# Performance work log

Measured on AMD Instinct MI355X. Metric: run time of the kernel, lower is better.

Reference implementation:

```python
import jax, jax.numpy as jnp
import numpy as np

H = 8
NEG = -1e9


def setup_inputs() -> dict:
    key = jax.random.key(0)
    ks = jax.random.split(key, 16)
    B, S, D = 4, 512, 512
    dk = D // H
    NUM_REL = 20 * 2 + 1  # 41
    s_in = 1.0 / np.sqrt(D)
    s_emb = np.sqrt(6.0 / (NUM_REL + dk))  # xavier_uniform
    inp = {
        "query": jax.random.normal(ks[0], (B, S, D), jnp.float32),
        "key": jax.random.normal(ks[1], (B, S, D), jnp.float32),
        "value": jax.random.normal(ks[2], (B, S, D), jnp.float32),
        "mask": jax.random.randint(ks[3], (B, S, S), 0, NUM_REL, jnp.int32),
        # linear layers stored as [in, out] (y = x @ W + b)
        "Wq": jax.random.normal(ks[4], (D, D), jnp.float32) * s_in,
        "bq": jnp.zeros((D,), jnp.float32),
        "Wk": jax.random.normal(ks[5], (D, D), jnp.float32) * s_in,
        "bk": jnp.zeros((D,), jnp.float32),
        "Wv": jax.random.normal(ks[6], (D, D), jnp.float32) * s_in,
        "bv": jnp.zeros((D,), jnp.float32),
        "Wo": jax.random.normal(ks[7], (D, D), jnp.float32) * s_in,
        "bo": jnp.zeros((D,), jnp.float32),
        "emb_k": jax.random.uniform(ks[8], (NUM_REL, dk), jnp.float32, -s_emb, s_emb),
        "emb_v": jax.random.uniform(ks[9], (NUM_REL, dk), jnp.float32, -s_emb, s_emb),
    }
    return inp


def reference(query, key, value, mask, Wq, bq, Wk, bk, Wv, bv, Wo, bo, emb_k, emb_v):
    B, Q, D = query.shape
    K = key.shape[1]
    dk = D // H
    # project and split heads -> [B, H, S, dk]
    q = (query @ Wq + bq).reshape(B, Q, H, dk).transpose(0, 2, 1, 3)
    k = (key @ Wk + bk).reshape(B, K, H, dk).transpose(0, 2, 1, 3)
    v = (value @ Wv + bv).reshape(B, K, H, dk).transpose(0, 2, 1, 3)
    # gather relative-position embeddings: [B, Q, K, dk]
    relem = emb_k[mask]
    relemv = emb_v[mask]
    scale = 1.0 / jnp.sqrt(jnp.asarray(dk, q.dtype))
    # content scores + relative-position bias scores
    scores = (jnp.einsum("bhqd,bhkd->bhqk", q, k)
              + jnp.einsum("bhqd,bqkd->bhqk", q, relem)) * scale
    # rmask = (mask > 0), broadcast over heads
    scores = jnp.where((mask > 0)[:, None, :, :], scores, NEG)
    attn = jax.nn.softmax(scores, axis=-1)
    # content values + relative-position value bias
    x = (jnp.einsum("bhqk,bhkd->bhqd", attn, v)
         + jnp.einsum("bhqk,bqkd->bhqd", attn, relemv))
    x = x.transpose(0, 2, 1, 3).reshape(B, Q, D)
    return x @ Wo + bo
```

## Files before the change

kernel.cpp:

```cpp
#include <hip/hip_runtime.h>

#define B_ 4
#define S_ 512
#define D_ 512
#define H_ 8
#define DK_ 64
#define NREL 41

typedef __attribute__((ext_vector_type(8))) short bf16x8;
typedef __attribute__((ext_vector_type(4))) float f32x4;

__device__ __forceinline__ unsigned short f2bf(float f) {
  unsigned u = __float_as_uint(f);
  u = u + 0x7FFFu + ((u >> 16) & 1u);
  return (unsigned short)(u >> 16);
}

#define MFMA16(a, b, c) __builtin_amdgcn_mfma_f32_16x16x32_bf16((a), (b), (c), 0, 0, 0)

struct PrepArgs { const float* W[4]; const float* in[3]; };

__global__ __launch_bounds__(256) void prep(PrepArgs PA,
    const float* __restrict__ embk, const float* __restrict__ embv,
    ushort* __restrict__ WT0, ushort* __restrict__ ekb, ushort* __restrict__ evt,
    ushort* __restrict__ inbf0)
{
  const int z = blockIdx.z;
  const int t = threadIdx.x;
  if (z == 4) {
    if (blockIdx.x || blockIdx.y) return;
    for (int i = t; i < 48 * 64; i += 256) {
      int r = i >> 6, d = i & 63;
      ekb[i] = (r < NREL) ? f2bf(embk[r * 64 + d]) : (ushort)0;
    }
    for (int i = t; i < 64 * 64; i += 256) {
      int d = i >> 6, r = i & 63;
      evt[i] = (r < NREL) ? f2bf(embv[r * 64 + d]) : (ushort)0;
    }
    return;
  }
  if (z >= 5) {
    const float* src = PA.in[z - 5];
    ushort* dst = inbf0 + (size_t)(z - 5) * ((size_t)2048 * 512);
    int lb = blockIdx.y * 8 + blockIdx.x;
    size_t base = (size_t)lb * 16384;
    #pragma unroll
    for (int i = 0; i < 16; ++i) {
      size_t off = base + (size_t)i * 1024 + t * 4;
      float4 v = *(const float4*)&src[off];
      ushort4 pk;
      pk.x = f2bf(v.x); pk.y = f2bf(v.y); pk.z = f2bf(v.z); pk.w = f2bf(v.w);
      *(ushort4*)&dst[off] = pk;
    }
    return;
  }
  __shared__ float sh[64][65];
  const float* W = PA.W[z];
  ushort* WT = WT0 + (size_t)z * (D_ * D_);
  const int k0 = blockIdx.x * 64, n0 = blockIdx.y * 64;
  const int rr = t >> 4, cc = (t & 15) * 4;
  #pragma unroll
  for (int i = 0; i < 4; ++i) {
    float4 v = *(const float4*)&W[(size_t)(k0 + rr + i * 16) * D_ + n0 + cc];
    sh[rr + i * 16][cc + 0] = v.x; sh[rr + i * 16][cc + 1] = v.y;
    sh[rr + i * 16][cc + 2] = v.z; sh[rr + i * 16][cc + 3] = v.w;
  }
  __syncthreads();
  #pragma unroll
  for (int i = 0; i < 4; ++i) {
    int r2 = rr + i * 16;
    ushort4 pk;
    pk.x = f2bf(sh[cc + 0][r2]); pk.y = f2bf(sh[cc + 1][r2]);
    pk.z = f2bf(sh[cc + 2][r2]); pk.w = f2bf(sh[cc + 3][r2]);
    *(ushort4*)&WT[(size_t)(n0 + r2) * D_ + k0 + cc] = pk;
  }
}

struct GemmP  { const ushort* A; const ushort* Wt; const float* bias; void* out; int mode; int kbeg; int kend; };
struct GemmPs { GemmP p[3]; };

__global__ __launch_bounds__(256) void gemm_bf16(GemmPs P)
{
  __shared__ ushort As[64][72];
  __shared__ ushort Bs[64][72];
  const GemmP gp = P.p[blockIdx.z];
  const int t = threadIdx.x, l = t & 63, w = t >> 6;
  const int r16 = l & 15, g4 = l >> 4;
  const int wmo = (w >> 1) * 32, wno = (w & 1) * 32;
  const int m0 = blockIdx.x * 64, n0 = blockIdx.y * 64;

  f32x4 acc[2][2];
  #pragma unroll
  for (int mi = 0; mi < 2; ++mi)
    #pragma unroll
    for (int ni = 0; ni < 2; ++ni) acc[mi][ni] = 0.0f;

  const int srow = t >> 2, sseg = (t & 3) * 16;
  for (int k0 = gp.kbeg; k0 < gp.kend; k0 += 64) {
    __syncthreads();
    *(uint4*)&As[srow][sseg]     = *(const uint4*)&gp.A[(size_t)(m0 + srow) * D_ + k0 + sseg];
    *(uint4*)&As[srow][sseg + 8] = *(const uint4*)&gp.A[(size_t)(m0 + srow) * D_ + k0 + sseg + 8];
    *(uint4*)&Bs[srow][sseg]     = *(const uint4*)&gp.Wt[(size_t)(n0 + srow) * D_ + k0 + sseg];
    *(uint4*)&Bs[srow][sseg + 8] = *(const uint4*)&gp.Wt[(size_t)(n0 + srow) * D_ + k0 + sseg + 8];
    __syncthreads();
    #pragma unroll
    for (int kk = 0; kk < 2; ++kk) {
      bf16x8 af[2], bfr[2];
      #pragma unroll
      for (int i = 0; i < 2; ++i) af[i]  = *(const bf16x8*)&As[wmo + i * 16 + r16][kk * 32 + g4 * 8];
      #pragma unroll
      for (int i = 0; i < 2; ++i) bfr[i] = *(const bf16x8*)&Bs[wno + i * 16 + r16][kk * 32 + g4 * 8];
      #pragma unroll
      for (int mi = 0; mi < 2; ++mi)
        #pragma unroll
        for (int ni = 0; ni < 2; ++ni)
          acc[mi][ni] = MFMA16(af[mi], bfr[ni], acc[mi][ni]);
    }
  }

  #pragma unroll
  for (int mi = 0; mi < 2; ++mi) {
    #pragma unroll
    for (int ni = 0; ni < 2; ++ni) {
      int n = n0 + wno + ni * 16 + r16;
      int mb = m0 + wmo + mi * 16 + g4 * 4;
      if (gp.mode == 3) {
        float* PO = (float*)gp.out;
        #pragma unroll
        for (int r = 0; r < 4; ++r) PO[(size_t)(mb + r) * D_ + n] = acc[mi][ni][r];
      } else {
        float bv = gp.bias[n];
        ushort* O = (ushort*)gp.out;
        int h = n >> 6, d = n & 63;
        if (gp.mode == 1) {
          #pragma unroll
          for (int r = 0; r < 4; ++r) {
            int m = mb + r, b = m >> 9, s = m & 511;
            O[(((size_t)(b * H_ + h)) * S_ + s) * DK_ + d] = f2bf(acc[mi][ni][r] + bv);
          }
        } else {
          int b = mb >> 9, s = mb & 511;
          ushort4 pk;
          pk.x = f2bf(acc[mi][ni][0] + bv); pk.y = f2bf(acc[mi][ni][1] + bv);
          pk.z = f2bf(acc[mi][ni][2] + bv); pk.w = f2bf(acc[mi][ni][3] + bv);
          *(ushort4*)&O[(((size_t)(b * H_ + h)) * DK_ + d) * S_ + s] = pk;
        }
      }
    }
  }
}

__global__ __launch_bounds__(64) void attn_mfma(
    const ushort* __restrict__ qb,
    const ushort* __restrict__ kb,
    const ushort* __restrict__ vtb,
    const int*    __restrict__ mask,
    const ushort* __restrict__ ekb,
    const ushort* __restrict__ evt,
    float* __restrict__ part,
    float* __restrict__ sums)
{
  __shared__ ushort Pb[16][72];
  __shared__ float qrel[16][48];
  __shared__ float wr[16][64];

  const int l = threadIdx.x;
  const int g = blockIdx.x;
  const int h = g & 7, b = (g >> 3) & 3;
  const int rest = g >> 5;
  const int chunk = rest & 3, qt = rest >> 2;
  const int bh = b * H_ + h;
  const int r16 = l & 15, g4 = l >> 4;

  for (int i = l; i < 16 * 64; i += 64) (&wr[0][0])[i] = 0.f;

  const size_t qoff = ((size_t)bh * S_ + qt * 16) * DK_;
  bf16x8 qf0 = *(const bf16x8*)&qb[qoff + (size_t)r16 * DK_ + g4 * 8];
  bf16x8 qf1 = *(const bf16x8*)&qb[qoff + (size_t)r16 * DK_ + 32 + g4 * 8];

  {
    #pragma unroll
    for (int s = 0; s < 3; ++s) {
      bf16x8 e0 = *(const bf16x8*)&ekb[(s * 16 + r16) * 64 + g4 * 8];
      bf16x8 e1 = *(const bf16x8*)&ekb[(s * 16 + r16) * 64 + 32 + g4 * 8];
      f32x4 qr = 0.0f;
      qr = MFMA16(qf0, e0, qr);
      qr = MFMA16(qf1, e1, qr);
      #pragma unroll
      for (int r = 0; r < 4; ++r) qrel[g4 * 4 + r][s * 16 + r16] = qr[r];
    }
  }
  __syncthreads();

  float ssum[4] = {0.f, 0.f, 0.f, 0.f};
  f32x4 oacc[4];
  #pragma unroll
  for (int i = 0; i < 4; ++i) oacc[i] = 0.0f;

  const int* mbase = mask + ((size_t)b * S_ + qt * 16) * S_;
  const size_t voff = (size_t)bh * DK_ * S_;

  const int kt0 = chunk * 2;
  for (int kt = kt0; kt < kt0 + 2; ++kt) {
    const size_t koff = ((size_t)bh * S_ + kt * 64) * DK_;
    f32x4 sacc[4];
    #pragma unroll
    for (int sub = 0; sub < 4; ++sub) {
      bf16x8 kf0 = *(const bf16x8*)&kb[koff + (size_t)(sub * 16 + r16) * DK_ + g4 * 8];
      bf16x8 kf1 = *(const bf16x8*)&kb[koff + (size_t)(sub * 16 + r16) * DK_ + 32 + g4 * 8];
      f32x4 z = 0.0f;
      z = MFMA16(qf0, kf0, z);
      z = MFMA16(qf1, kf1, z);
      sacc[sub] = z;
    }
    #pragma unroll
    for (int sub = 0; sub < 4; ++sub) {
      #pragma unroll
      for (int r = 0; r < 4; ++r) {
        int row = g4 * 4 + r;
        int col = kt * 64 + sub * 16 + r16;
        int mv = mbase[(size_t)row * S_ + col];
        float sc = (sacc[sub][r] + qrel[row][mv]) * 0.125f;
        float e = (mv > 0) ? __expf(sc) : 0.f;
        ssum[r] += e;
        atomicAdd(&wr[row][mv], e);
        Pb[row][sub * 16 + r16] = f2bf(e);
      }
    }
    __syncthreads();
    bf16x8 pf0 = *(const bf16x8*)&Pb[r16][g4 * 8];
    bf16x8 pf1 = *(const bf16x8*)&Pb[r16][32 + g4 * 8];
    #pragma unroll
    for (int ds = 0; ds < 4; ++ds) {
      bf16x8 vf0 = *(const bf16x8*)&vtb[voff + (size_t)(ds * 16 + r16) * S_ + kt * 64 + g4 * 8];
      bf16x8 vf1 = *(const bf16x8*)&vtb[voff + (size_t)(ds * 16 + r16) * S_ + kt * 64 + 32 + g4 * 8];
      oacc[ds] = MFMA16(pf0, vf0, oacc[ds]);
      oacc[ds] = MFMA16(pf1, vf1, oacc[ds]);
    }
    __syncthreads();
  }

  for (int i = 0; i < 16; ++i) Pb[r16][g4 * 16 + i] = f2bf(wr[r16][g4 * 16 + i]);
  __syncthreads();
  {
    bf16x8 wf0 = *(const bf16x8*)&Pb[r16][g4 * 8];
    bf16x8 wf1 = *(const bf16x8*)&Pb[r16][32 + g4 * 8];
    #pragma unroll
    for (int ds = 0; ds < 4; ++ds) {
      bf16x8 e0 = *(const bf16x8*)&evt[(ds * 16 + r16) * 64 + g4 * 8];
      bf16x8 e1 = *(const bf16x8*)&evt[(ds * 16 + r16) * 64 + 32 + g4 * 8];
      oacc[ds] = MFMA16(wf0, e0, oacc[ds]);
      oacc[ds] = MFMA16(wf1, e1, oacc[ds]);
    }
  }

  #pragma unroll
  for (int m = 1; m < 16; m <<= 1)
    #pragma unroll
    for (int r = 0; r < 4; ++r) ssum[r] += __shfl_xor(ssum[r], m);

  #pragma unroll
  for (int r = 0; r < 4; ++r) {
    int q = qt * 16 + g4 * 4 + r;
    float* dst = part + (((size_t)chunk * B_ + b) * S_ + q) * D_ + h * DK_;
    #pragma unroll
    for (int ds = 0; ds < 4; ++ds) dst[ds * 16 + r16] = oacc[ds][r];
  }
  if (r16 == 0) {
    size_t sb = ((size_t)chunk * 32 + bh) * S_ + qt * 16 + g4 * 4;
    sums[sb + 0] = ssum[0]; sums[sb + 1] = ssum[1];
    sums[sb + 2] = ssum[2]; sums[sb + 3] = ssum[3];
  }
}

__global__ __launch_bounds__(256) void attn_reduce(
    const float* __restrict__ part, const float* __restrict__ sums,
    ushort* __restrict__ ctx)
{
  int idx = blockIdx.x * 256 + threadIdx.x;
  int d4 = idx & 127;
  int s  = (idx >> 7) & 511;
  int b  = idx >> 16;
  int h  = d4 >> 4;
  float sm = 0.f;
  #pragma unroll
  for (int c = 0; c < 4; ++c) sm += sums[((size_t)c * 32 + b * 8 + h) * S_ + s];
  float inv = 1.f / sm;
  float4 o = make_float4(0.f, 0.f, 0.f, 0.f);
  #pragma unroll
  for (int c = 0; c < 4; ++c) {
    float4 p = *(const float4*)&part[(((size_t)c * B_ + b) * S_ + s) * D_ + d4 * 4];
    o.x += p.x; o.y += p.y; o.z += p.z; o.w += p.w;
  }
  ushort4 pk;
  pk.x = f2bf(o.x * inv); pk.y = f2bf(o.y * inv);
  pk.z = f2bf(o.z * inv); pk.w = f2bf(o.w * inv);
  *(ushort4*)&ctx[((size_t)b * S_ + s) * D_ + d4 * 4] = pk;
}

__global__ __launch_bounds__(256) void out_reduce(
    const float* __restrict__ po, const float* __restrict__ bo,
    float* __restrict__ out)
{
  int idx = blockIdx.x * 256 + threadIdx.x;
  int n4 = (idx & 127) * 4;
  size_t off = (size_t)idx * 4;
  float4 a = *(const float4*)&po[off];
  float4 c = *(const float4*)&po[off + (size_t)2048 * 512];
  float4 bb = *(const float4*)&bo[n4];
  float4 o = make_float4(a.x + c.x + bb.x, a.y + c.y + bb.y,
                         a.z + c.z + bb.z, a.w + c.w + bb.w);
  *(float4*)&out[off] = o;
}

extern "C" void kernel_launch(void* const* d_in, const int* in_sizes, int n_in,
                              void* d_out, int out_size, void* d_ws, size_t ws_size,
                              hipStream_t stream) {
  (void)in_sizes; (void)n_in; (void)out_size; (void)ws_size;
  const float* query = (const float*)d_in[0];
  const float* key   = (const float*)d_in[1];
  const float* value = (const float*)d_in[2];
  const int*   mask  = (const int*)d_in[3];
  const float* Wq = (const float*)d_in[4];
  const float* bq = (const float*)d_in[5];
  const float* Wk = (const float*)d_in[6];
  const float* bk = (const float*)d_in[7];
  const float* Wv = (const float*)d_in[8];
  const float* bv = (const float*)d_in[9];
  const float* Wo = (const float*)d_in[10];
  const float* bo = (const float*)d_in[11];
  const float* embk = (const float*)d_in[12];
  const float* embv = (const float*)d_in[13];
  float* out = (float*)d_out;

  const size_t MD  = (size_t)2048 * 512;
  const size_t WSZ = (size_t)D_ * D_;
  ushort* wsu  = (ushort*)d_ws;
  ushort* WT   = wsu;
  ushort* ekb  = WT + 4 * WSZ;
  ushort* evt  = ekb + 3072;
  ushort* qbf  = evt + 4096;
  ushort* kbf  = qbf + MD;
  ushort* vtbf = kbf + MD;
  ushort* ctx  = vtbf + MD;
  ushort* inbf = ctx + MD;
  float*  sums = (float*)(inbf + 3 * MD);
  float*  part = sums + (size_t)4 * 32 * 512;
  float*  po   = part;

  PrepArgs PA;
  PA.W[0] = Wq; PA.W[1] = Wk; PA.W[2] = Wv; PA.W[3] = Wo;
  PA.in[0] = query; PA.in[1] = key; PA.in[2] = value;
  prep<<<dim3(8, 8, 8), 256, 0, stream>>>(PA, embk, embv, WT, ekb, evt, inbf);

  GemmPs P1;
  P1.p[0] = { inbf,          WT + 0 * WSZ, bq, qbf,  1, 0, 512 };
  P1.p[1] = { inbf + MD,     WT + 1 * WSZ, bk, kbf,  1, 0, 512 };
  P1.p[2] = { inbf + 2 * MD, WT + 2 * WSZ, bv, vtbf, 2, 0, 512 };
  gemm_bf16<<<dim3(32, 8, 3), 256, 0, stream>>>(P1);

  attn_mfma<<<dim3(4096), 64, 0, stream>>>(qbf, kbf, vtbf, mask, ekb, evt, part, sums);
  attn_reduce<<<dim3(1024), 256, 0, stream>>>(part, sums, ctx);

  GemmPs P2;
  P2.p[0] = { ctx, WT + 3 * WSZ, nullptr, po,      3, 0,   256 };
  P2.p[1] = { ctx, WT + 3 * WSZ, nullptr, po + MD, 3, 256, 512 };
  P2.p[2] = P2.p[0];
  gemm_bf16<<<dim3(32, 8, 2), 256, 0, stream>>>(P2);

  out_reduce<<<dim3(1024), 256, 0, stream>>>(po, bo, out);
}
```

Measured before the change: 189.2 us.

## Pack mask to bytes, fold scale into Q, batch 4 q-tiles per block

The prep kernel now converts the int32 relative-position mask to uint8, so attention reads a quarter of the mask bytes. The 1/sqrt(dk) scale is folded into the Q projection epilogue, which removes the per-score multiply. Attention blocks now run four independent 64-thread waves, one q-tile each, with per-wave LDS slices. The __syncthreads calls become a waitcnt fence, and the K, V and mask loads are hoisted ahead of compute. The risks are extra prep work, wave-local fencing that depends on single-wave LDS ownership, and a prep pass of mask conversion that is paid on every call.

```diff
diff --git a/kernel.cpp b/kernel.cpp
--- a/kernel.cpp
+++ b/kernel.cpp
@@ -18,24 +18,41 @@
 
 #define MFMA16(a, b, c) __builtin_amdgcn_mfma_f32_16x16x32_bf16((a), (b), (c), 0, 0, 0)
 
+#define LDS_FENCE() do { \
+  asm volatile("s_waitcnt lgkmcnt(0)" ::: "memory"); \
+  __builtin_amdgcn_sched_barrier(0); \
+} while (0)
+
 struct PrepArgs { const float* W[4]; const float* in[3]; };
 
 __global__ __launch_bounds__(256) void prep(PrepArgs PA,
     const float* __restrict__ embk, const float* __restrict__ embv,
+    const int* __restrict__ mask,
     ushort* __restrict__ WT0, ushort* __restrict__ ekb, ushort* __restrict__ evt,
-    ushort* __restrict__ inbf0)
+    ushort* __restrict__ inbf0, uchar* __restrict__ mask8)
 {
   const int z = blockIdx.z;
   const int t = threadIdx.x;
   if (z == 4) {
-    if (blockIdx.x || blockIdx.y) return;
-    for (int i = t; i < 48 * 64; i += 256) {
-      int r = i >> 6, d = i & 63;
-      ekb[i] = (r < NREL) ? f2bf(embk[r * 64 + d]) : (ushort)0;
-    }
-    for (int i = t; i < 64 * 64; i += 256) {
-      int d = i >> 6, r = i & 63;
-      evt[i] = (r < NREL) ? f2bf(embv[r * 64 + d]) : (ushort)0;
+    int lb = blockIdx.y * 8 + blockIdx.x;
+    size_t base = (size_t)lb * 16384;
+    #pragma unroll
+    for (int i = 0; i < 16; ++i) {
+      size_t off = base + (size_t)i * 1024 + t * 4;
+      int4 v = *(const int4*)&mask[off];
+      uchar4 pk;
+      pk.x = (uchar)v.x; pk.y = (uchar)v.y; pk.z = (uchar)v.z; pk.w = (uchar)v.w;
+      *(uchar4*)&mask8[off] = pk;
+    }
+    if (lb == 0) {
+      for (int i = t; i < 48 * 64; i += 256) {
+        int r = i >> 6, d = i & 63;
+        ekb[i] = (r < NREL) ? f2bf(embk[r * 64 + d]) : (ushort)0;
+      }
+      for (int i = t; i < 64 * 64; i += 256) {
+        int d = i >> 6, r = i & 63;
+        evt[i] = (r < NREL) ? f2bf(embv[r * 64 + d]) : (ushort)0;
+      }
     }
     return;
   }
@@ -76,7 +93,8 @@
   }
 }
 
-struct GemmP  { const ushort* A; const ushort* Wt; const float* bias; void* out; int mode; int kbeg; int kend; };
+struct GemmP  { const ushort* A; const ushort* Wt; const float* bias; void* out;
+                int mode; int kbeg; int kend; float oscale; };
 struct GemmPs { GemmP p[3]; };
 
 __global__ __launch_bounds__(256) void gemm_bf16(GemmPs P)
@@ -136,7 +154,7 @@
           #pragma unroll
           for (int r = 0; r < 4; ++r) {
             int m = mb + r, b = m >> 9, s = m & 511;
-            O[(((size_t)(b * H_ + h)) * S_ + s) * DK_ + d] = f2bf(acc[mi][ni][r] + bv);
+            O[(((size_t)(b * H_ + h)) * S_ + s) * DK_ + d] = f2bf((acc[mi][ni][r] + bv) * gp.oscale);
           }
         } else {
           int b = mb >> 9, s = mb & 511;
@@ -150,29 +168,34 @@
   }
 }
 
-__global__ __launch_bounds__(64) void attn_mfma(
+__global__ __launch_bounds__(256) void attn_mfma(
     const ushort* __restrict__ qb,
     const ushort* __restrict__ kb,
     const ushort* __restrict__ vtb,
-    const int*    __restrict__ mask,
+    const uchar* __restrict__ mask8,
     const ushort* __restrict__ ekb,
     const ushort* __restrict__ evt,
     float* __restrict__ part,
     float* __restrict__ sums)
 {
-  __shared__ ushort Pb[16][72];
-  __shared__ float qrel[16][48];
-  __shared__ float wr[16][64];
-
-  const int l = threadIdx.x;
+  __shared__ float  qrelS[4][16][48];
+  __shared__ float  wrS[4][16][44];
+  __shared__ ushort PbS[4][16][72];
+  const int t = threadIdx.x, w = t >> 6, l = t & 63;
   const int g = blockIdx.x;
-  const int h = g & 7, b = (g >> 3) & 3;
-  const int rest = g >> 5;
-  const int chunk = rest & 3, qt = rest >> 2;
+  const int h = g & 7, b = (g >> 3) & 3, chunk = (g >> 5) & 3, qtg = g >> 7;
+  const int qt = qtg * 4 + w;
   const int bh = b * H_ + h;
   const int r16 = l & 15, g4 = l >> 4;
-
-  for (int i = l; i < 16 * 64; i += 64) (&wr[0][0])[i] = 0.f;
+  float  (*qrel)[48] = qrelS[w];
+  float  (*wr)[44]   = wrS[w];
+  ushort (*Pb)[72]   = PbS[w];
+
+  {
+    float* wrf = &wr[0][0];
+    #pragma unroll
+    for (int i = 0; i < 11; ++i) wrf[i * 64 + l] = 0.f;
+  }
 
   const size_t qoff = ((size_t)bh * S_ + qt * 16) * DK_;
   bf16x8 qf0 = *(const bf16x8*)&qb[qoff + (size_t)r16 * DK_ + g4 * 8];
@@ -190,58 +213,78 @@
       for (int r = 0; r < 4; ++r) qrel[g4 * 4 + r][s * 16 + r16] = qr[r];
     }
   }
-  __syncthreads();
+  LDS_FENCE();
 
   float ssum[4] = {0.f, 0.f, 0.f, 0.f};
   f32x4 oacc[4];
   #pragma unroll
   for (int i = 0; i < 4; ++i) oacc[i] = 0.0f;
 
-  const int* mbase = mask + ((size_t)b * S_ + qt * 16) * S_;
+  const uchar* mbase = mask8 + ((size_t)b * S_ + qt * 16) * S_;
   const size_t voff = (size_t)bh * DK_ * S_;
-
   const int kt0 = chunk * 2;
-  for (int kt = kt0; kt < kt0 + 2; ++kt) {
+
+  #pragma unroll
+  for (int kti = 0; kti < 2; ++kti) {
+    const int kt = kt0 + kti;
     const size_t koff = ((size_t)bh * S_ + kt * 64) * DK_;
+    bf16x8 kf0[4], kf1[4];
+    #pragma unroll
+    for (int sub = 0; sub < 4; ++sub) {
+      kf0[sub] = *(const bf16x8*)&kb[koff + (size_t)(sub * 16 + r16) * DK_ + g4 * 8];
+      kf1[sub] = *(const bf16x8*)&kb[koff + (size_t)(sub * 16 + r16) * DK_ + 32 + g4 * 8];
+    }
     f32x4 sacc[4];
     #pragma unroll
     for (int sub = 0; sub < 4; ++sub) {
-      bf16x8 kf0 = *(const bf16x8*)&kb[koff + (size_t)(sub * 16 + r16) * DK_ + g4 * 8];
-      bf16x8 kf1 = *(const bf16x8*)&kb[koff + (size_t)(sub * 16 + r16) * DK_ + 32 + g4 * 8];
       f32x4 z = 0.0f;
-      z = MFMA16(qf0, kf0, z);
-      z = MFMA16(qf1, kf1, z);
+      z = MFMA16(qf0, kf0[sub], z);
+      z = MFMA16(qf1, kf1[sub], z);
       sacc[sub] = z;
     }
+    bf16x8 vf0[4], vf1[4];
+    #pragma unroll
+    for (int ds = 0; ds < 4; ++ds) {
+      vf0[ds] = *(const bf16x8*)&vtb[voff + (size_t)(ds * 16 + r16) * S_ + kt * 64 + g4 * 8];
+      vf1[ds] = *(const bf16x8*)&vtb[voff + (size_t)(ds * 16 + r16) * S_ + kt * 64 + 32 + g4 * 8];
+    }
+    int mv[16];
+    #pragma unroll
+    for (int sub = 0; sub < 4; ++sub)
+      #pragma unroll
+      for (int r = 0; r < 4; ++r)
+        mv[sub * 4 + r] = mbase[(size_t)(g4 * 4 + r) * S_ + kt * 64 + sub * 16 + r16];
+    float qv[16];
+    #pragma unroll
+    for (int i = 0; i < 16; ++i) qv[i] = qrel[g4 * 4 + (i & 3)][mv[i]];
     #pragma unroll
     for (int sub = 0; sub < 4; ++sub) {
       #pragma unroll
       for (int r = 0; r < 4; ++r) {
-        int row = g4 * 4 + r;
-        int col = kt * 64 + sub * 16 + r16;
-        int mv = mbase[(size_t)row * S_ + col];
-        float sc = (sacc[sub][r] + qrel[row][mv]) * 0.125f;
-        float e = (mv > 0) ? __expf(sc) : 0.f;
+        int i = sub * 4 + r;
+        float e = (mv[i] > 0) ? __expf(sacc[sub][r] + qv[i]) : 0.f;
         ssum[r] += e;
-        atomicAdd(&wr[row][mv], e);
-        Pb[row][sub * 16 + r16] = f2bf(e);
+        atomicAdd(&wr[g4 * 4 + r][mv[i]], e);
+        Pb[g4 * 4 + r][sub * 16 + r16] = f2bf(e);
       }
     }
-    __syncthreads();
+    LDS_FENCE();
     bf16x8 pf0 = *(const bf16x8*)&Pb[r16][g4 * 8];
     bf16x8 pf1 = *(const bf16x8*)&Pb[r16][32 + g4 * 8];
+    LDS_FENCE();
     #pragma unroll
     for (int ds = 0; ds < 4; ++ds) {
-      bf16x8 vf0 = *(const bf16x8*)&vtb[voff + (size_t)(ds * 16 + r16) * S_ + kt * 64 + g4 * 8];
-      bf16x8 vf1 = *(const bf16x8*)&vtb[voff + (size_t)(ds * 16 + r16) * S_ + kt * 64 + 32 + g4 * 8];
-      oacc[ds] = MFMA16(pf0, vf0, oacc[ds]);
-      oacc[ds] = MFMA16(pf1, vf1, oacc[ds]);
-    }
-    __syncthreads();
-  }
-
-  for (int i = 0; i < 16; ++i) Pb[r16][g4 * 16 + i] = f2bf(wr[r16][g4 * 16 + i]);
-  __syncthreads();
+      oacc[ds] = MFMA16(pf0, vf0[ds], oacc[ds]);
+      oacc[ds] = MFMA16(pf1, vf1[ds], oacc[ds]);
+    }
+  }
+
+  #pragma unroll
+  for (int i = 0; i < 16; ++i) {
+    int col = g4 * 16 + i;
+    Pb[r16][col] = (col < 44) ? f2bf(wr[r16][col]) : (ushort)0;
+  }
+  LDS_FENCE();
   {
     bf16x8 wf0 = *(const bf16x8*)&Pb[r16][g4 * 8];
     bf16x8 wf1 = *(const bf16x8*)&Pb[r16][32 + g4 * 8];
@@ -347,24 +390,25 @@
   float*  sums = (float*)(inbf + 3 * MD);
   float*  part = sums + (size_t)4 * 32 * 512;
   float*  po   = part;
+  uchar*  mask8 = (uchar*)(part + 4 * MD);
 
   PrepArgs PA;
   PA.W[0] = Wq; PA.W[1] = Wk; PA.W[2] = Wv; PA.W[3] = Wo;
   PA.in[0] = query; PA.in[1] = key; PA.in[2] = value;
-  prep<<<dim3(8, 8, 8), 256, 0, stream>>>(PA, embk, embv, WT, ekb, evt, inbf);
+  prep<<<dim3(8, 8, 8), 256, 0, stream>>>(PA, embk, embv, mask, WT, ekb, evt, inbf, mask8);
 
   GemmPs P1;
-  P1.p[0] = { inbf,          WT + 0 * WSZ, bq, qbf,  1, 0, 512 };
-  P1.p[1] = { inbf + MD,     WT + 1 * WSZ, bk, kbf,  1, 0, 512 };
-  P1.p[2] = { inbf + 2 * MD, WT + 2 * WSZ, bv, vtbf, 2, 0, 512 };
+  P1.p[0] = { inbf,          WT + 0 * WSZ, bq, qbf,  1, 0, 512, 0.125f };
+  P1.p[1] = { inbf + MD,     WT + 1 * WSZ, bk, kbf,  1, 0, 512, 1.0f };
+  P1.p[2] = { inbf + 2 * MD, WT + 2 * WSZ, bv, vtbf, 2, 0, 512, 1.0f };
   gemm_bf16<<<dim3(32, 8, 3), 256, 0, stream>>>(P1);
 
-  attn_mfma<<<dim3(4096), 64, 0, stream>>>(qbf, kbf, vtbf, mask, ekb, evt, part, sums);
+  attn_mfma<<<dim3(1024), 256, 0, stream>>>(qbf, kbf, vtbf, mask8, ekb, evt, part, sums);
   attn_reduce<<<dim3(1024), 256, 0, stream>>>(part, sums, ctx);
 
   GemmPs P2;
-  P2.p[0] = { ctx, WT + 3 * WSZ, nullptr, po,      3, 0,   256 };
-  P2.p[1] = { ctx, WT + 3 * WSZ, nullptr, po + MD, 3, 256, 512 };
+  P2.p[0] = { ctx, WT + 3 * WSZ, nullptr, po,      3, 0,   256, 1.0f };
+  P2.p[1] = { ctx, WT + 3 * WSZ, nullptr, po + MD, 3, 256, 512, 1.0f };
   P2.p[2] = P2.p[0];
   gemm_bf16<<<dim3(32, 8, 2), 256, 0, stream>>>(P2);
 
```

Result: faster. 180.6 us (-4.5%).
